# Performance work log

Hardware: AMD Instinct MI355X
Metric: run time of the kernel (lower is better)

Reference implementation:

```python
import jax, jax.numpy as jnp
import numpy as np

B = 2
D_MODEL = 256
D_FFN = 1024
N_LEVELS = 4
N_HEADS = 8
N_POINTS = 4
D_HEAD = D_MODEL // N_HEADS
SHAPES = np.array([[128, 128], [64, 64], [32, 32], [16, 16]], dtype=np.int32)  # (H, W) per level
LEN = int(SHAPES.prod(axis=1).sum())  # 21760
EPS = 1e-5


def _layer_norm(x, g, b):
    m = jnp.mean(x, axis=-1, keepdims=True)
    v = jnp.mean(jnp.square(x - m), axis=-1, keepdims=True)
    return (x - m) * jax.lax.rsqrt(v + EPS) * g + b


def _bilinear_gather(v_l, loc, H, W):
    # v_l: [B, H*W, NH, DH]; loc: [B, L, NH, NP, 2] in normalized [0,1] coords (x, y)
    # grid_sample(align_corners=False, padding_mode=zeros) semantics: pixel = loc * size - 0.5
    x = loc[..., 0] * W - 0.5
    y = loc[..., 1] * H - 0.5
    x0 = jnp.floor(x)
    y0 = jnp.floor(y)
    dx = x - x0
    dy = y - y0
    x0i = x0.astype(jnp.int32)
    y0i = y0.astype(jnp.int32)
    b_ix = jnp.arange(v_l.shape[0])[:, None, None, None]
    h_ix = jnp.arange(v_l.shape[2])[None, None, :, None]

    def corner(xi, yi, w):
        valid = (xi >= 0) & (xi < W) & (yi >= 0) & (yi < H)
        idx = jnp.clip(yi, 0, H - 1) * W + jnp.clip(xi, 0, W - 1)
        v = v_l[b_ix, idx, h_ix]  # [B, L, NH, NP, DH]
        return v * (w * valid.astype(v.dtype))[..., None]

    return (corner(x0i, y0i, (1 - dx) * (1 - dy))
            + corner(x0i + 1, y0i, dx * (1 - dy))
            + corner(x0i, y0i + 1, (1 - dx) * dy)
            + corner(x0i + 1, y0i + 1, dx * dy))


def _forward(src, pos, reference_points,
             w_off, b_off, w_attn, b_attn, w_val, b_val, w_out, b_out,
             ln1_g, ln1_b, w1, b1, w2, b2, ln2_g, ln2_b,
             spatial_shapes, level_start_index, padding_mask):
    shapes = np.asarray(spatial_shapes)        # static per-level (H, W)
    starts = np.asarray(level_start_index)     # static level offsets
    Bsz, L, _ = src.shape

    # ---- MSDeformAttn ----
    q = src + pos                              # with_pos_embed
    value = src @ w_val + b_val
    value = jnp.where(padding_mask[..., None], 0.0, value)
    value = value.reshape(Bsz, L, N_HEADS, D_HEAD)

    off = (q @ w_off + b_off).reshape(Bsz, L, N_HEADS, N_LEVELS, N_POINTS, 2)
    attn = (q @ w_attn + b_attn).reshape(Bsz, L, N_HEADS, N_LEVELS * N_POINTS)
    attn = jax.nn.softmax(attn, axis=-1).reshape(Bsz, L, N_HEADS, N_LEVELS, N_POINTS)

    wh = jnp.asarray(shapes[:, ::-1].copy(), dtype=src.dtype)  # [NL, 2] = (W, H)
    loc = reference_points[:, :, None, :, None, :] + off / wh[None, None, None, :, None, :]

    out = jnp.zeros((Bsz, L, N_HEADS, D_HEAD), src.dtype)
    for l in range(N_LEVELS):
        H, W = int(shapes[l, 0]), int(shapes[l, 1])
        s = int(starts[l])
        v_l = value[:, s:s + H * W]                          # [B, H*W, NH, DH]
        sampled = _bilinear_gather(v_l, loc[:, :, :, l], H, W)  # [B, L, NH, NP, DH]
        out = out + (sampled * attn[:, :, :, l][..., None]).sum(axis=3)
    attn_out = out.reshape(Bsz, L, D_MODEL) @ w_out + b_out

    # ---- residual + LN + FFN + residual + LN (dropout = identity in eval) ----
    x = _layer_norm(src + attn_out, ln1_g, ln1_b)
    ffn = jax.nn.relu(x @ w1 + b1) @ w2 + b2
    return _layer_norm(x + ffn, ln2_g, ln2_b)


def setup_inputs() -> dict:
    key = jax.random.key(0)
    ks = jax.random.split(key, 16)
    s = 0.02
    n_off = N_HEADS * N_LEVELS * N_POINTS
    level_start = np.concatenate([[0], SHAPES.prod(axis=1).cumsum()[:-1]]).astype(np.int32)
    return {
        "src": jax.random.normal(ks[0], (B, LEN, D_MODEL), jnp.float32),
        "pos": jax.random.normal(ks[1], (B, LEN, D_MODEL), jnp.float32),
        "reference_points": jax.random.uniform(ks[2], (B, LEN, N_LEVELS, 2), jnp.float32),
        "spatial_shapes": jnp.asarray(SHAPES),
        "level_start_index": jnp.asarray(level_start),
        "padding_mask": jnp.zeros((B, LEN), jnp.bool_),
        "w_off": jax.random.normal(ks[3], (D_MODEL, n_off * 2), jnp.float32) * s,
        "b_off": jax.random.normal(ks[4], (n_off * 2,), jnp.float32) * 0.5,
        "w_attn": jax.random.normal(ks[5], (D_MODEL, n_off), jnp.float32) * s,
        "b_attn": jnp.zeros((n_off,), jnp.float32),
        "w_val": jax.random.normal(ks[6], (D_MODEL, D_MODEL), jnp.float32) * s,
        "b_val": jnp.zeros((D_MODEL,), jnp.float32),
        "w_out": jax.random.normal(ks[7], (D_MODEL, D_MODEL), jnp.float32) * s,
        "b_out": jnp.zeros((D_MODEL,), jnp.float32),
        "ln1_g": jnp.ones((D_MODEL,), jnp.float32),
        "ln1_b": jnp.zeros((D_MODEL,), jnp.float32),
        "w1": jax.random.normal(ks[8], (D_MODEL, D_FFN), jnp.float32) * s,
        "b1": jnp.zeros((D_FFN,), jnp.float32),
        "w2": jax.random.normal(ks[9], (D_FFN, D_MODEL), jnp.float32) * s,
        "b2": jnp.zeros((D_MODEL,), jnp.float32),
        "ln2_g": jnp.ones((D_MODEL,), jnp.float32),
        "ln2_b": jnp.zeros((D_MODEL,), jnp.float32),
    }


def reference(src, pos, reference_points, spatial_shapes, level_start_index, padding_mask,
              w_off, b_off, w_attn, b_attn, w_val, b_val, w_out, b_out,
              ln1_g, ln1_b, w1, b1, w2, b2, ln2_g, ln2_b):
    return _forward(src, pos, reference_points,
                    w_off, b_off, w_attn, b_attn, w_val, b_val, w_out, b_out,
                    ln1_g, ln1_b, w1, b1, w2, b2, ln2_g, ln2_b,
                    spatial_shapes, level_start_index, padding_mask)
```

## Files before the change

### kernel.cpp

```cpp
#include <hip/hip_runtime.h>
#include <hip/hip_bf16.h>

#define BSZ      2
#define LTOK     21760
#define NTOK     (BSZ * LTOK)
#define DMODEL   256
#define DFFN     1024

typedef __attribute__((ext_vector_type(8))) short short8;
typedef __attribute__((ext_vector_type(4))) float f32x4;

__device__ __forceinline__ unsigned short f2bf(float x) {
    __hip_bfloat16 h = __float2bfloat16(x);
    return *reinterpret_cast<unsigned short*>(&h);
}
__device__ __forceinline__ float bf2f(unsigned short u) {
    union { unsigned int i; float f; } c; c.i = ((unsigned int)u) << 16; return c.f;
}
__device__ __forceinline__ float bflo(unsigned int u) {
    union { unsigned int i; float f; } c; c.i = u << 16; return c.f;
}
__device__ __forceinline__ float bfhi(unsigned int u) {
    union { unsigned int i; float f; } c; c.i = u & 0xffff0000u; return c.f;
}

#define TM 128
#define TN 128
#define TBK 32
#define EBS 132

__global__ __launch_bounds__(256) void gemm_mfma(
    const void* __restrict__ Av, const float* __restrict__ A2,
    const unsigned short* __restrict__ Bt, const float* __restrict__ bias,
    unsigned short* __restrict__ Cb,
    int M, int N, int K, int amode, int relu, int cmode,
    const unsigned char* __restrict__ mask)
{
    __shared__ __align__(16) unsigned short smem[TM * TBK + TN * TBK];
    unsigned short* sA = smem;
    unsigned short* sB = smem + TM * TBK;

    const int tid  = threadIdx.x;
    const int lane = tid & 63;
    const int wave = tid >> 6;
    const int wm = wave >> 1, wn = wave & 1;

    const int bm = blockIdx.y * TM;
    const int bn = blockIdx.x * TN;

    const int sr = tid >> 6;
    const int fr = lane & 15;
    const int fk = (lane >> 4) * 8;

    f32x4 acc[4][4];
    #pragma unroll
    for (int i = 0; i < 4; ++i)
        #pragma unroll
        for (int j = 0; j < 4; ++j)
            acc[i][j] = (f32x4){0.f, 0.f, 0.f, 0.f};

    for (int k0 = 0; k0 < K; k0 += TBK) {
        #pragma unroll
        for (int rr = 0; rr < 2; ++rr) {
            const int s = sr + rr * 4;
            const size_t grow = (size_t)(bm + s * 16 + fr);
            unsigned short* dst = &sA[s * 512 + lane * 8];
            if (amode == 0) {
                const float* Af = (const float*)Av + grow * K + k0 + fk;
                float4 v0 = *(const float4*)Af;
                float4 v1 = *(const float4*)(Af + 4);
                if (A2) {
                    const float* Pf = A2 + grow * K + k0 + fk;
                    const float4 p0 = *(const float4*)Pf;
                    const float4 p1 = *(const float4*)(Pf + 4);
                    v0.x += p0.x; v0.y += p0.y; v0.z += p0.z; v0.w += p0.w;
                    v1.x += p1.x; v1.y += p1.y; v1.z += p1.z; v1.w += p1.w;
                }
                const unsigned int p0 = (unsigned)f2bf(v0.x) | ((unsigned)f2bf(v0.y) << 16);
                const unsigned int p1 = (unsigned)f2bf(v0.z) | ((unsigned)f2bf(v0.w) << 16);
                const unsigned int p2 = (unsigned)f2bf(v1.x) | ((unsigned)f2bf(v1.y) << 16);
                const unsigned int p3 = (unsigned)f2bf(v1.z) | ((unsigned)f2bf(v1.w) << 16);
                *(uint4*)dst = make_uint4(p0, p1, p2, p3);
            } else {
                const unsigned short* Ab = (const unsigned short*)Av + grow * K + k0 + fk;
                *(uint4*)dst = *(const uint4*)Ab;
            }
        }
        #pragma unroll
        for (int rr = 0; rr < 2; ++rr) {
            const int s = sr + rr * 4;
            const size_t gn = (size_t)(bn + s * 16 + fr);
            *(uint4*)&sB[s * 512 + lane * 8] = *(const uint4*)(Bt + gn * K + k0 + fk);
        }
        __syncthreads();

        short8 af[4], bfr[4];
        #pragma unroll
        for (int i = 0; i < 4; ++i)
            af[i] = *(const short8*)&sA[(wm * 4 + i) * 512 + lane * 8];
        #pragma unroll
        for (int j = 0; j < 4; ++j)
            bfr[j] = *(const short8*)&sB[(wn * 4 + j) * 512 + lane * 8];
        #pragma unroll
        for (int i = 0; i < 4; ++i)
            #pragma unroll
            for (int j = 0; j < 4; ++j)
                acc[i][j] = __builtin_amdgcn_mfma_f32_16x16x32_bf16(
                    af[i], bfr[j], acc[i][j], 0, 0, 0);
        __syncthreads();
    }

    const int r0 = (lane >> 4) * 4;
    const int c0 = lane & 15;
    unsigned short* eb = smem;

    #pragma unroll
    for (int i = 0; i < 4; ++i) {
        if (i) __syncthreads();
        #pragma unroll
        for (int j = 0; j < 4; ++j) {
            const int col = bn + wn * 64 + j * 16 + c0;
            const float bj = bias ? bias[col] : 0.f;
            #pragma unroll
            for (int r = 0; r < 4; ++r) {
                const int row = bm + wm * 64 + i * 16 + r0 + r;
                float v = acc[i][j][r] + bj;
                if (relu) v = fmaxf(v, 0.f);
                if (mask && mask[row]) v = 0.f;
                eb[(wm * 16 + r0 + r) * EBS + wn * 64 + j * 16 + c0] = f2bf(v);
            }
        }
        __syncthreads();
        #pragma unroll
        for (int qq = 0; qq < 2; ++qq) {
            const int q  = tid + qq * 256;
            const int rl = q >> 4;
            const int ch = q & 15;
            const int grow = bm + (rl >> 4) * 64 + i * 16 + (rl & 15);
            const uint4 val = *(const uint4*)&eb[rl * EBS + ch * 8];
            if (cmode == 1) {
                const int bb   = grow >= LTOK;
                const int srow = grow - bb * LTOK;
                const int hcol = (bn + ch * 8) >> 5;
                const int d    = (ch & 3) * 8;
                *(uint4*)&Cb[((size_t)(bb * 8 + hcol) * LTOK + srow) * 32 + d] = val;
            } else {
                *(uint4*)&Cb[(size_t)grow * N + bn + ch * 8] = val;
            }
        }
    }
}

__global__ void transpose_cast(const float* __restrict__ W,
                               unsigned short* __restrict__ Wt, int K, int N)
{
    __shared__ float t[32][33];
    const int k0 = blockIdx.x * 32, n0 = blockIdx.y * 32;
    const int tx = threadIdx.x, ty = threadIdx.y;
    #pragma unroll
    for (int i = 0; i < 32; i += 8)
        t[ty + i][tx] = W[(size_t)(k0 + ty + i) * N + n0 + tx];
    __syncthreads();
    #pragma unroll
    for (int i = 0; i < 32; i += 8)
        Wt[(size_t)(n0 + ty + i) * K + k0 + tx] = f2bf(t[tx][ty + i]);
}

__global__ void concat_bias(const float* __restrict__ b_off,
                            const float* __restrict__ b_att,
                            float* __restrict__ dst)
{
    const int t = threadIdx.x;
    dst[t] = (t < 256) ? b_off[t] : b_att[t - 256];
}

__global__ __launch_bounds__(256) void sample_kernel(
    const unsigned short* __restrict__ vT, const unsigned short* __restrict__ qp,
    const float* __restrict__ ref,
    const int* __restrict__ sshapes, const int* __restrict__ lstart,
    unsigned short* __restrict__ samp)
{
    __shared__ float s_w[256][4];
    __shared__ int   s_o[256][4];

    const int blk   = blockIdx.x;
    const int plane = blk & 15;
    const int chunk = blk >> 4;
    const int b = plane >> 3;
    const int h = plane & 7;
    const int s0 = chunk * 16;
    const int t = threadIdx.x;

    {
        const int tl = t >> 4;
        const int p  = t & 15;
        const int l  = p >> 2;
        const int pp = p & 3;
        const int H = sshapes[2 * l], W = sshapes[2 * l + 1];
        const float Wf = (float)W, Hf = (float)H;
        const size_t tok = (size_t)(b * LTOK + s0 + tl);

        const float ox = bf2f(qp[tok * 384 + h * 32 + l * 8 + pp * 2 + 0]);
        const float oy = bf2f(qp[tok * 384 + h * 32 + l * 8 + pp * 2 + 1]);
        const float rx = ref[tok * 8 + l * 2 + 0];
        const float ry = ref[tok * 8 + l * 2 + 1];

        const float x = (rx + ox / Wf) * Wf - 0.5f;
        const float y = (ry + oy / Hf) * Hf - 0.5f;
        const float x0 = floorf(x), y0 = floorf(y);
        const float dx = x - x0, dy = y - y0;
        const int x0i = (int)x0, y0i = (int)y0;
        const int s = lstart[l];

        const float a = bf2f(qp[tok * 384 + 256 + h * 16 + p]);
        float mx = a;
        #pragma unroll
        for (int m = 8; m; m >>= 1) mx = fmaxf(mx, __shfl_xor(mx, m, 16));
        const float e = __expf(a - mx);
        float ssum = e;
        #pragma unroll
        for (int m = 8; m; m >>= 1) ssum += __shfl_xor(ssum, m, 16);
        const float prob = e / ssum;

        const float cw[4] = {(1.f - dx) * (1.f - dy), dx * (1.f - dy),
                             (1.f - dx) * dy,         dx * dy};
        const int cx[4] = {x0i, x0i + 1, x0i,     x0i + 1};
        const int cy[4] = {y0i, y0i,     y0i + 1, y0i + 1};
        #pragma unroll
        for (int c = 0; c < 4; ++c) {
            const bool valid = (cx[c] >= 0) & (cx[c] < W) & (cy[c] >= 0) & (cy[c] < H);
            const int xi = min(max(cx[c], 0), W - 1);
            const int yi = min(max(cy[c], 0), H - 1);
            s_o[t][c] = (s + yi * W + xi) * 64;
            s_w[t][c] = valid ? cw[c] * prob : 0.f;
        }
    }
    __syncthreads();

    const int tl = t >> 4;
    const int dp = t & 15;
    const char* vp = (const char*)(vT + (size_t)plane * LTOK * 32) + dp * 4;
    float acc0 = 0.f, acc1 = 0.f;
    #pragma unroll
    for (int p = 0; p < 16; ++p) {
        const int sl = tl * 16 + p;
        #pragma unroll
        for (int c = 0; c < 4; ++c) {
            const float w = s_w[sl][c];
            const unsigned int u = *(const unsigned int*)(vp + s_o[sl][c]);
            acc0 = fmaf(w, bflo(u), acc0);
            acc1 = fmaf(w, bfhi(u), acc1);
        }
    }
    const unsigned int o = (unsigned)f2bf(acc0) | ((unsigned)f2bf(acc1) << 16);
    *(unsigned int*)(samp + (size_t)(b * LTOK + s0 + tl) * 256 + h * 32 + dp * 2) = o;
}

__global__ __launch_bounds__(256) void ln_kernel(
    const void* __restrict__ a, int a_bf16,
    const void* __restrict__ b, int b_bf16,
    const float* __restrict__ g, const float* __restrict__ be,
    float* __restrict__ outF, unsigned short* __restrict__ outB)
{
    const int wid  = threadIdx.x >> 6;
    const int lane = threadIdx.x & 63;
    const int tok  = blockIdx.x * 4 + wid;
    const size_t base = (size_t)tok * 256 + lane * 4;

    float4 va, vb;
    if (a_bf16) {
        const ushort4 u = *(const ushort4*)((const unsigned short*)a + base);
        va.x = bf2f(u.x); va.y = bf2f(u.y); va.z = bf2f(u.z); va.w = bf2f(u.w);
    } else {
        va = *(const float4*)((const float*)a + base);
    }
    if (b_bf16) {
        const ushort4 u = *(const ushort4*)((const unsigned short*)b + base);
        vb.x = bf2f(u.x); vb.y = bf2f(u.y); vb.z = bf2f(u.z); vb.w = bf2f(u.w);
    } else {
        vb = *(const float4*)((const float*)b + base);
    }
    float4 v;
    v.x = va.x + vb.x; v.y = va.y + vb.y; v.z = va.z + vb.z; v.w = va.w + vb.w;

    float s  = v.x + v.y + v.z + v.w;
    float sq = v.x * v.x + v.y * v.y + v.z * v.z + v.w * v.w;
    #pragma unroll
    for (int m = 32; m; m >>= 1) {
        s  += __shfl_xor(s, m, 64);
        sq += __shfl_xor(sq, m, 64);
    }
    const float mean = s * (1.f / 256.f);
    const float var  = sq * (1.f / 256.f) - mean * mean;
    const float rs   = rsqrtf(var + 1e-5f);

    const float4 g4 = *(const float4*)(g + lane * 4);
    const float4 b4 = *(const float4*)(be + lane * 4);
    float4 o;
    o.x = (v.x - mean) * rs * g4.x + b4.x;
    o.y = (v.y - mean) * rs * g4.y + b4.y;
    o.z = (v.z - mean) * rs * g4.z + b4.z;
    o.w = (v.w - mean) * rs * g4.w + b4.w;
    if (outF) *(float4*)(outF + base) = o;
    if (outB) {
        ushort4 u;
        u.x = f2bf(o.x); u.y = f2bf(o.y); u.z = f2bf(o.z); u.w = f2bf(o.w);
        *(ushort4*)(outB + base) = u;
    }
}

extern "C" void kernel_launch(void* const* d_in, const int* in_sizes, int n_in,
                              void* d_out, int out_size, void* d_ws, size_t ws_size,
                              hipStream_t stream)
{
    const float* src   = (const float*)d_in[0];
    const float* pos   = (const float*)d_in[1];
    const float* ref   = (const float*)d_in[2];
    const int*   sshap = (const int*)d_in[3];
    const int*   lstrt = (const int*)d_in[4];
    const unsigned char* mask = (const unsigned char*)d_in[5];
    const float* w_off = (const float*)d_in[6];
    const float* b_off = (const float*)d_in[7];
    const float* w_att = (const float*)d_in[8];
    const float* b_att = (const float*)d_in[9];
    const float* w_val = (const float*)d_in[10];
    const float* b_val = (const float*)d_in[11];
    const float* w_out = (const float*)d_in[12];
    const float* b_out = (const float*)d_in[13];
    const float* ln1g  = (const float*)d_in[14];
    const float* ln1b  = (const float*)d_in[15];
    const float* w1    = (const float*)d_in[16];
    const float* b1    = (const float*)d_in[17];
    const float* w2    = (const float*)d_in[18];
    const float* b2    = (const float*)d_in[19];
    const float* ln2g  = (const float*)d_in[20];
    const float* ln2b  = (const float*)d_in[21];
    float* out = (float*)d_out;

    const size_t SZB = (size_t)NTOK * 256 * 4;
    char* w = (char*)d_ws;
    unsigned short* qpb    = (unsigned short*)w;
    unsigned short* aof16  = (unsigned short*)w;
    unsigned short* hidb   = (unsigned short*)w;
    unsigned short* vT     = (unsigned short*)(w + SZB * 3 / 2);
    unsigned short* samp16 = (unsigned short*)(w + SZB * 2);
    unsigned short* ffb    = samp16;
    unsigned short* xb     = (unsigned short*)(w + SZB * 2 + SZB / 2);
    char* wreg = w + SZB * 3;
    unsigned short* wvalT  = (unsigned short*)wreg;
    unsigned short* woaT   = wvalT + 256 * 256;
    unsigned short* woutT  = woaT + 384 * 256;
    unsigned short* w1T    = woutT + 256 * 256;
    unsigned short* w2T    = w1T + 1024 * 256;
    float*          bcat   = (float*)(w2T + 256 * 1024);

    const dim3 blk(256);
    const dim3 tblk(32, 8);

    transpose_cast<<<dim3(8, 8),  tblk, 0, stream>>>(w_val, wvalT, 256, 256);
    transpose_cast<<<dim3(8, 8),  tblk, 0, stream>>>(w_off, woaT,  256, 256);
    transpose_cast<<<dim3(8, 4),  tblk, 0, stream>>>(w_att, woaT + 256 * 256, 256, 128);
    transpose_cast<<<dim3(8, 8),  tblk, 0, stream>>>(w_out, woutT, 256, 256);
    transpose_cast<<<dim3(8, 32), tblk, 0, stream>>>(w1,    w1T,   256, 1024);
    transpose_cast<<<dim3(32, 8), tblk, 0, stream>>>(w2,    w2T,   1024, 256);
    concat_bias<<<1, 384, 0, stream>>>(b_off, b_att, bcat);

    gemm_mfma<<<dim3(2, NTOK / TM), blk, 0, stream>>>(
        src, nullptr, wvalT, b_val, vT, NTOK, 256, 256, 0, 0, 1, mask);
    gemm_mfma<<<dim3(3, NTOK / TM), blk, 0, stream>>>(
        src, pos, woaT, bcat, qpb, NTOK, 384, 256, 0, 0, 0, nullptr);

    sample_kernel<<<dim3(16 * (LTOK / 16)), blk, 0, stream>>>(
        vT, qpb, ref, sshap, lstrt, samp16);

    gemm_mfma<<<dim3(2, NTOK / TM), blk, 0, stream>>>(
        samp16, nullptr, woutT, b_out, aof16, NTOK, 256, 256, 1, 0, 0, nullptr);

    ln_kernel<<<dim3(NTOK / 4), blk, 0, stream>>>(
        src, 0, aof16, 1, ln1g, ln1b, nullptr, xb);

    gemm_mfma<<<dim3(8, NTOK / TM), blk, 0, stream>>>(
        xb, nullptr, w1T, b1, hidb, NTOK, DFFN, 256, 1, 1, 0, nullptr);
    gemm_mfma<<<dim3(2, NTOK / TM), blk, 0, stream>>>(
        hidb, nullptr, w2T, b2, ffb, NTOK, 256, DFFN, 1, 0, 0, nullptr);

    ln_kernel<<<dim3(NTOK / 4), blk, 0, stream>>>(
        xb, 1, ffb, 1, ln2g, ln2b, out, nullptr);
}
```

Measured before the change: 522.9 us.

## Widen GEMM tile to 256 columns, precast inputs to bf16, merge weight transposes

```diff
diff --git a/kernel.cpp b/kernel.cpp
--- a/kernel.cpp
+++ b/kernel.cpp
@@ -25,15 +25,15 @@
 }
 
 #define TM 128
-#define TN 128
+#define TN 256
 #define TBK 32
-#define EBS 132
-
-__global__ __launch_bounds__(256) void gemm_mfma(
-    const void* __restrict__ Av, const float* __restrict__ A2,
+#define EBS 264
+
+__global__ __launch_bounds__(256, 2) void gemm_mfma(
+    const unsigned short* __restrict__ A,
     const unsigned short* __restrict__ Bt, const float* __restrict__ bias,
     unsigned short* __restrict__ Cb,
-    int M, int N, int K, int amode, int relu, int cmode,
+    int M, int N, int K, int relu, int cmode,
     const unsigned char* __restrict__ mask)
 {
     __shared__ __align__(16) unsigned short smem[TM * TBK + TN * TBK];
@@ -52,11 +52,11 @@
     const int fr = lane & 15;
     const int fk = (lane >> 4) * 8;
 
-    f32x4 acc[4][4];
+    f32x4 acc[4][8];
     #pragma unroll
     for (int i = 0; i < 4; ++i)
         #pragma unroll
-        for (int j = 0; j < 4; ++j)
+        for (int j = 0; j < 8; ++j)
             acc[i][j] = (f32x4){0.f, 0.f, 0.f, 0.f};
 
     for (int k0 = 0; k0 < K; k0 += TBK) {
@@ -64,47 +64,28 @@
         for (int rr = 0; rr < 2; ++rr) {
             const int s = sr + rr * 4;
             const size_t grow = (size_t)(bm + s * 16 + fr);
-            unsigned short* dst = &sA[s * 512 + lane * 8];
-            if (amode == 0) {
-                const float* Af = (const float*)Av + grow * K + k0 + fk;
-                float4 v0 = *(const float4*)Af;
-                float4 v1 = *(const float4*)(Af + 4);
-                if (A2) {
-                    const float* Pf = A2 + grow * K + k0 + fk;
-                    const float4 p0 = *(const float4*)Pf;
-                    const float4 p1 = *(const float4*)(Pf + 4);
-                    v0.x += p0.x; v0.y += p0.y; v0.z += p0.z; v0.w += p0.w;
-                    v1.x += p1.x; v1.y += p1.y; v1.z += p1.z; v1.w += p1.w;
-                }
-                const unsigned int p0 = (unsigned)f2bf(v0.x) | ((unsigned)f2bf(v0.y) << 16);
-                const unsigned int p1 = (unsigned)f2bf(v0.z) | ((unsigned)f2bf(v0.w) << 16);
-                const unsigned int p2 = (unsigned)f2bf(v1.x) | ((unsigned)f2bf(v1.y) << 16);
-                const unsigned int p3 = (unsigned)f2bf(v1.z) | ((unsigned)f2bf(v1.w) << 16);
-                *(uint4*)dst = make_uint4(p0, p1, p2, p3);
-            } else {
-                const unsigned short* Ab = (const unsigned short*)Av + grow * K + k0 + fk;
-                *(uint4*)dst = *(const uint4*)Ab;
-            }
-        }
-        #pragma unroll
-        for (int rr = 0; rr < 2; ++rr) {
+            *(uint4*)&sA[s * 512 + lane * 8] = *(const uint4*)(A + grow * K + k0 + fk);
+        }
+        #pragma unroll
+        for (int rr = 0; rr < 4; ++rr) {
             const int s = sr + rr * 4;
-            const size_t gn = (size_t)(bn + s * 16 + fr);
-            *(uint4*)&sB[s * 512 + lane * 8] = *(const uint4*)(Bt + gn * K + k0 + fk);
+            int gn = bn + s * 16 + fr;
+            gn = min(gn, N - 1);
+            *(uint4*)&sB[s * 512 + lane * 8] = *(const uint4*)(Bt + (size_t)gn * K + k0 + fk);
         }
         __syncthreads();
 
-        short8 af[4], bfr[4];
+        short8 af[4], bfr[8];
         #pragma unroll
         for (int i = 0; i < 4; ++i)
             af[i] = *(const short8*)&sA[(wm * 4 + i) * 512 + lane * 8];
         #pragma unroll
-        for (int j = 0; j < 4; ++j)
-            bfr[j] = *(const short8*)&sB[(wn * 4 + j) * 512 + lane * 8];
+        for (int j = 0; j < 8; ++j)
+            bfr[j] = *(const short8*)&sB[(wn * 8 + j) * 512 + lane * 8];
         #pragma unroll
         for (int i = 0; i < 4; ++i)
             #pragma unroll
-            for (int j = 0; j < 4; ++j)
+            for (int j = 0; j < 8; ++j)
                 acc[i][j] = __builtin_amdgcn_mfma_f32_16x16x32_bf16(
                     af[i], bfr[j], acc[i][j], 0, 0, 0);
         __syncthreads();
@@ -118,45 +99,87 @@
     for (int i = 0; i < 4; ++i) {
         if (i) __syncthreads();
         #pragma unroll
-        for (int j = 0; j < 4; ++j) {
-            const int col = bn + wn * 64 + j * 16 + c0;
-            const float bj = bias ? bias[col] : 0.f;
+        for (int j = 0; j < 8; ++j) {
+            const int col = bn + wn * 128 + j * 16 + c0;
+            const float bj = (col < N) ? bias[col] : 0.f;
             #pragma unroll
             for (int r = 0; r < 4; ++r) {
                 const int row = bm + wm * 64 + i * 16 + r0 + r;
                 float v = acc[i][j][r] + bj;
                 if (relu) v = fmaxf(v, 0.f);
                 if (mask && mask[row]) v = 0.f;
-                eb[(wm * 16 + r0 + r) * EBS + wn * 64 + j * 16 + c0] = f2bf(v);
+                eb[(wm * 16 + r0 + r) * EBS + wn * 128 + j * 16 + c0] = f2bf(v);
             }
         }
         __syncthreads();
         #pragma unroll
-        for (int qq = 0; qq < 2; ++qq) {
+        for (int qq = 0; qq < 4; ++qq) {
             const int q  = tid + qq * 256;
-            const int rl = q >> 4;
-            const int ch = q & 15;
+            const int rl = q >> 5;
+            const int ch = q & 31;
             const int grow = bm + (rl >> 4) * 64 + i * 16 + (rl & 15);
-            const uint4 val = *(const uint4*)&eb[rl * EBS + ch * 8];
-            if (cmode == 1) {
-                const int bb   = grow >= LTOK;
-                const int srow = grow - bb * LTOK;
-                const int hcol = (bn + ch * 8) >> 5;
-                const int d    = (ch & 3) * 8;
-                *(uint4*)&Cb[((size_t)(bb * 8 + hcol) * LTOK + srow) * 32 + d] = val;
-            } else {
-                *(uint4*)&Cb[(size_t)grow * N + bn + ch * 8] = val;
+            const int colb = bn + ch * 8;
+            if (colb < N) {
+                const uint4 val = *(const uint4*)&eb[rl * EBS + ch * 8];
+                if (cmode == 1) {
+                    const int bb   = grow >= LTOK;
+                    const int srow = grow - bb * LTOK;
+                    const int hcol = ch >> 2;
+                    const int d    = (ch & 3) * 8;
+                    *(uint4*)&Cb[((size_t)(bb * 8 + hcol) * LTOK + srow) * 32 + d] = val;
+                } else {
+                    *(uint4*)&Cb[(size_t)grow * N + colb] = val;
+                }
             }
         }
     }
 }
 
-__global__ void transpose_cast(const float* __restrict__ W,
-                               unsigned short* __restrict__ Wt, int K, int N)
-{
+__global__ __launch_bounds__(256) void prepass(
+    const float* __restrict__ src, const float* __restrict__ pos,
+    unsigned short* __restrict__ sb, unsigned short* __restrict__ qs)
+{
+    const size_t i = ((size_t)blockIdx.x * 256 + threadIdx.x) * 4;
+    const float4 s = *(const float4*)(src + i);
+    const float4 p = *(const float4*)(pos + i);
+    ushort4 us, uq;
+    us.x = f2bf(s.x); us.y = f2bf(s.y); us.z = f2bf(s.z); us.w = f2bf(s.w);
+    uq.x = f2bf(s.x + p.x); uq.y = f2bf(s.y + p.y);
+    uq.z = f2bf(s.z + p.z); uq.w = f2bf(s.w + p.w);
+    *(ushort4*)(sb + i) = us;
+    *(ushort4*)(qs + i) = uq;
+}
+
+__global__ void transpose_all(
+    const float* __restrict__ w_val, const float* __restrict__ w_off,
+    const float* __restrict__ w_att, const float* __restrict__ w_out,
+    const float* __restrict__ w1,    const float* __restrict__ w2,
+    const float* __restrict__ b_off, const float* __restrict__ b_att,
+    unsigned short* __restrict__ wvalT, unsigned short* __restrict__ woaT,
+    unsigned short* __restrict__ woutT, unsigned short* __restrict__ w1T,
+    unsigned short* __restrict__ w2T,   float* __restrict__ bcat)
+{
+    const int blk = blockIdx.x;
+    const int tx = threadIdx.x, ty = threadIdx.y;
+    if (blk == 736) {
+        const int t = ty * 32 + tx;
+        bcat[t] = (t < 256) ? b_off[t] : b_att[t - 256];
+        if (t + 256 < 384) bcat[t + 256] = b_att[t + 256 - 256];
+        return;
+    }
+    const float* W; unsigned short* Wt; int K, N, base;
+    if      (blk < 64)  { W = w_val; Wt = wvalT;           K = 256;  N = 256;  base = 0;   }
+    else if (blk < 128) { W = w_off; Wt = woaT;            K = 256;  N = 256;  base = 64;  }
+    else if (blk < 160) { W = w_att; Wt = woaT + 256*256;  K = 256;  N = 128;  base = 128; }
+    else if (blk < 224) { W = w_out; Wt = woutT;           K = 256;  N = 256;  base = 160; }
+    else if (blk < 480) { W = w1;    Wt = w1T;             K = 256;  N = 1024; base = 224; }
+    else                { W = w2;    Wt = w2T;             K = 1024; N = 256;  base = 480; }
+    const int local = blk - base;
+    const int kb = local % (K / 32);
+    const int nb = local / (K / 32);
+    const int k0 = kb * 32, n0 = nb * 32;
+
     __shared__ float t[32][33];
-    const int k0 = blockIdx.x * 32, n0 = blockIdx.y * 32;
-    const int tx = threadIdx.x, ty = threadIdx.y;
     #pragma unroll
     for (int i = 0; i < 32; i += 8)
         t[ty + i][tx] = W[(size_t)(k0 + ty + i) * N + n0 + tx];
@@ -164,14 +187,6 @@
     #pragma unroll
     for (int i = 0; i < 32; i += 8)
         Wt[(size_t)(n0 + ty + i) * K + k0 + tx] = f2bf(t[tx][ty + i]);
-}
-
-__global__ void concat_bias(const float* __restrict__ b_off,
-                            const float* __restrict__ b_att,
-                            float* __restrict__ dst)
-{
-    const int t = threadIdx.x;
-    dst[t] = (t < 256) ? b_off[t] : b_att[t - 256];
 }
 
 __global__ __launch_bounds__(256) void sample_kernel(
@@ -180,8 +195,8 @@
     const int* __restrict__ sshapes, const int* __restrict__ lstart,
     unsigned short* __restrict__ samp)
 {
-    __shared__ float s_w[256][4];
-    __shared__ int   s_o[256][4];
+    __shared__ float s_w[4][256];
+    __shared__ int   s_o[4][256];
 
     const int blk   = blockIdx.x;
     const int plane = blk & 15;
@@ -231,8 +246,8 @@
             const bool valid = (cx[c] >= 0) & (cx[c] < W) & (cy[c] >= 0) & (cy[c] < H);
             const int xi = min(max(cx[c], 0), W - 1);
             const int yi = min(max(cy[c], 0), H - 1);
-            s_o[t][c] = (s + yi * W + xi) * 64;
-            s_w[t][c] = valid ? cw[c] * prob : 0.f;
+            s_o[c][t] = (s + yi * W + xi) * 64;
+            s_w[c][t] = valid ? cw[c] * prob : 0.f;
         }
     }
     __syncthreads();
@@ -246,8 +261,8 @@
         const int sl = tl * 16 + p;
         #pragma unroll
         for (int c = 0; c < 4; ++c) {
-            const float w = s_w[sl][c];
-            const unsigned int u = *(const unsigned int*)(vp + s_o[sl][c]);
+            const float w = s_w[c][sl];
+            const unsigned int u = *(const unsigned int*)(vp + s_o[c][sl]);
             acc0 = fmaf(w, bflo(u), acc0);
             acc1 = fmaf(w, bfhi(u), acc1);
         }
@@ -257,8 +272,7 @@
 }
 
 __global__ __launch_bounds__(256) void ln_kernel(
-    const void* __restrict__ a, int a_bf16,
-    const void* __restrict__ b, int b_bf16,
+    const unsigned short* __restrict__ a, const unsigned short* __restrict__ b,
     const float* __restrict__ g, const float* __restrict__ be,
     float* __restrict__ outF, unsigned short* __restrict__ outB)
 {
@@ -267,21 +281,13 @@
     const int tok  = blockIdx.x * 4 + wid;
     const size_t base = (size_t)tok * 256 + lane * 4;
 
-    float4 va, vb;
-    if (a_bf16) {
-        const ushort4 u = *(const ushort4*)((const unsigned short*)a + base);
-        va.x = bf2f(u.x); va.y = bf2f(u.y); va.z = bf2f(u.z); va.w = bf2f(u.w);
-    } else {
-        va = *(const float4*)((const float*)a + base);
-    }
-    if (b_bf16) {
-        const ushort4 u = *(const ushort4*)((const unsigned short*)b + base);
-        vb.x = bf2f(u.x); vb.y = bf2f(u.y); vb.z = bf2f(u.z); vb.w = bf2f(u.w);
-    } else {
-        vb = *(const float4*)((const float*)b + base);
-    }
+    const ushort4 ua = *(const ushort4*)(a + base);
+    const ushort4 ub = *(const ushort4*)(b + base);
     float4 v;
-    v.x = va.x + vb.x; v.y = va.y + vb.y; v.z = va.z + vb.z; v.w = va.w + vb.w;
+    v.x = bf2f(ua.x) + bf2f(ub.x);
+    v.y = bf2f(ua.y) + bf2f(ub.y);
+    v.z = bf2f(ua.z) + bf2f(ub.z);
+    v.w = bf2f(ua.w) + bf2f(ub.w);
 
     float s  = v.x + v.y + v.z + v.w;
     float sq = v.x * v.x + v.y * v.y + v.z * v.z + v.w * v.w;
@@ -337,16 +343,18 @@
     const float* ln2b  = (const float*)d_in[21];
     float* out = (float*)d_out;
 
-    const size_t SZB = (size_t)NTOK * 256 * 4;
+    const size_t HSZ = (size_t)NTOK * 256 * 2;
     char* w = (char*)d_ws;
-    unsigned short* qpb    = (unsigned short*)w;
-    unsigned short* aof16  = (unsigned short*)w;
+    unsigned short* qs     = (unsigned short*)w;
+    unsigned short* samp16 = (unsigned short*)w;
+    unsigned short* qpb    = (unsigned short*)(w + HSZ);
+    unsigned short* vT     = (unsigned short*)(w + HSZ * 5 / 2);
+    unsigned short* aof16  = (unsigned short*)(w + HSZ * 7 / 2);
     unsigned short* hidb   = (unsigned short*)w;
-    unsigned short* vT     = (unsigned short*)(w + SZB * 3 / 2);
-    unsigned short* samp16 = (unsigned short*)(w + SZB * 2);
-    unsigned short* ffb    = samp16;
-    unsigned short* xb     = (unsigned short*)(w + SZB * 2 + SZB / 2);
-    char* wreg = w + SZB * 3;
+    unsigned short* sb     = (unsigned short*)(w + HSZ * 9 / 2);
+    unsigned short* ffb    = sb;
+    unsigned short* xb     = (unsigned short*)(w + HSZ * 11 / 2);
+    char* wreg = w + HSZ * 13 / 2;
     unsigned short* wvalT  = (unsigned short*)wreg;
     unsigned short* woaT   = wvalT + 256 * 256;
     unsigned short* woutT  = woaT + 384 * 256;
@@ -355,35 +363,34 @@
     float*          bcat   = (float*)(w2T + 256 * 1024);
 
     const dim3 blk(256);
-    const dim3 tblk(32, 8);
-
-    transpose_cast<<<dim3(8, 8),  tblk, 0, stream>>>(w_val, wvalT, 256, 256);
-    transpose_cast<<<dim3(8, 8),  tblk, 0, stream>>>(w_off, woaT,  256, 256);
-    transpose_cast<<<dim3(8, 4),  tblk, 0, stream>>>(w_att, woaT + 256 * 256, 256, 128);
-    transpose_cast<<<dim3(8, 8),  tblk, 0, stream>>>(w_out, woutT, 256, 256);
-    transpose_cast<<<dim3(8, 32), tblk, 0, stream>>>(w1,    w1T,   256, 1024);
-    transpose_cast<<<dim3(32, 8), tblk, 0, stream>>>(w2,    w2T,   1024, 256);
-    concat_bias<<<1, 384, 0, stream>>>(b_off, b_att, bcat);
+
+    prepass<<<dim3(NTOK / 4), blk, 0, stream>>>(src, pos, sb, qs);
+
+    transpose_all<<<dim3(737), dim3(32, 8), 0, stream>>>(
+        w_val, w_off, w_att, w_out, w1, w2, b_off, b_att,
+        wvalT, woaT, woutT, w1T, w2T, bcat);
+
+    gemm_mfma<<<dim3(1, NTOK / TM), blk, 0, stream>>>(
+        sb, wvalT, b_val, vT, NTOK, 256, 256, 0, 1, mask);
 
     gemm_mfma<<<dim3(2, NTOK / TM), blk, 0, stream>>>(
-        src, nullptr, wvalT, b_val, vT, NTOK, 256, 256, 0, 0, 1, mask);
-    gemm_mfma<<<dim3(3, NTOK / TM), blk, 0, stream>>>(
-        src, pos, woaT, bcat, qpb, NTOK, 384, 256, 0, 0, 0, nullptr);
+        qs, woaT, bcat, qpb, NTOK, 384, 256, 0, 0, nullptr);
 
     sample_kernel<<<dim3(16 * (LTOK / 16)), blk, 0, stream>>>(
         vT, qpb, ref, sshap, lstrt, samp16);
 
-    gemm_mfma<<<dim3(2, NTOK / TM), blk, 0, stream>>>(
-        samp16, nullptr, woutT, b_out, aof16, NTOK, 256, 256, 1, 0, 0, nullptr);
+    gemm_mfma<<<dim3(1, NTOK / TM), blk, 0, stream>>>(
+        samp16, woutT, b_out, aof16, NTOK, 256, 256, 0, 0, nullptr);
 
     ln_kernel<<<dim3(NTOK / 4), blk, 0, stream>>>(
-        src, 0, aof16, 1, ln1g, ln1b, nullptr, xb);
-
-    gemm_mfma<<<dim3(8, NTOK / TM), blk, 0, stream>>>(
-        xb, nullptr, w1T, b1, hidb, NTOK, DFFN, 256, 1, 1, 0, nullptr);
-    gemm_mfma<<<dim3(2, NTOK / TM), blk, 0, stream>>>(
-        hidb, nullptr, w2T, b2, ffb, NTOK, 256, DFFN, 1, 0, 0, nullptr);
+        sb, aof16, ln1g, ln1b, nullptr, xb);
+
+    gemm_mfma<<<dim3(4, NTOK / TM), blk, 0, stream>>>(
+        xb, w1T, b1, hidb, NTOK, DFFN, 256, 1, 0, nullptr);
+
+    gemm_mfma<<<dim3(1, NTOK / TM), blk, 0, stream>>>(
+        hidb, w2T, b2, ffb, NTOK, 256, DFFN, 0, 0, nullptr);
 
     ln_kernel<<<dim3(NTOK / 4), blk, 0, stream>>>(
-        xb, 1, ffb, 1, ln2g, ln2b, out, nullptr);
-}
+        xb, ffb, ln2g, ln2b, out, nullptr);
+}
```

Result: slower. 562.2 us (+7.5%).
